# Kernel optimization log

Hardware: AMD Instinct MI355X
Metric: run time of the kernel (lower is better)

Reference implementation:

```python
import jax, jax.numpy as jnp
import numpy as np

HEADS = 16
HEAD_DIM = 64  # embed_size 1024 // 16


def setup_inputs() -> dict:
    key = jax.random.key(0)
    ks = jax.random.split(key, 6)
    N, S, E = 2, 2048, 1024
    return {
        "values": jax.random.normal(ks[0], (N, S, E), dtype=jnp.float32),
        "keys": jax.random.normal(ks[1], (N, S, E), dtype=jnp.float32),
        "queries": jax.random.normal(ks[2], (N, S, E), dtype=jnp.float32),
        "Wv": jax.random.normal(ks[3], (E, E), dtype=jnp.float32) * (E ** -0.5),
        "Wk": jax.random.normal(ks[4], (E, E), dtype=jnp.float32) * (E ** -0.5),
        "Wq": jax.random.normal(ks[5], (E, E), dtype=jnp.float32) * (E ** -0.5),
    }


def reference(values, keys, queries, Wv, Wk, Wq):
    N, Sq, E = queries.shape
    Sk = keys.shape[1]
    H, D = HEADS, HEAD_DIM
    # linear projections (torch Linear: x @ W^T), then split heads
    v = (values @ Wv.T).reshape(N, Sk, H, D)
    k = (keys @ Wk.T).reshape(N, Sk, H, D)
    q = (queries @ Wq.T).reshape(N, Sq, H, D)
    # QK^T -> [N, H, Q, K]
    scores = jnp.einsum("nqhd,nkhd->nhqk", q, k)
    # no mask (original forward takes mask=None path); scale by sqrt(head_dim)
    attn = jax.nn.softmax(scores / jnp.asarray(D, scores.dtype) ** 0.5, axis=-1)
    # AV -> [N, Q, H, D] -> [N, Q, E]; note: fc_out is never applied in the original forward
    out = jnp.einsum("nhql,nlhd->nqhd", attn, v).reshape(N, Sq, H * D)
    return out
```

## Files before the change

### kernel.cpp

```cpp
#include <hip/hip_runtime.h>
#include <math.h>

#define SEQ 2048
#define EMB 1024
#define NH  16
#define HD  64

typedef __attribute__((ext_vector_type(8))) short short8;
typedef __attribute__((ext_vector_type(4))) float f32x4;

static const size_t XE = (size_t)2 * SEQ * EMB;
static const size_t WE = (size_t)EMB * EMB;

static __device__ __forceinline__ short f2bf(float f) {
    unsigned u = __builtin_bit_cast(unsigned, f);
    u = u + 0x7fffu + ((u >> 16) & 1u);
    return (short)(u >> 16);
}

#if __has_builtin(__builtin_amdgcn_cvt_pk_bf16_f32)
typedef __attribute__((ext_vector_type(2))) __bf16 bf16x2;
static __device__ __forceinline__ unsigned pk2(float a, float b) {
    bf16x2 v = __builtin_amdgcn_cvt_pk_bf16_f32(a, b);
    return __builtin_bit_cast(unsigned, v);
}
#else
static __device__ __forceinline__ unsigned pk2(float a, float b) {
    return (unsigned)(unsigned short)f2bf(a) |
           ((unsigned)(unsigned short)f2bf(b) << 16);
}
#endif

static __device__ __forceinline__ short8 cvt8(float4 a, float4 b) {
    union { unsigned u[4]; short8 s; } r;
    r.u[0] = pk2(a.x, a.y); r.u[1] = pk2(a.z, a.w);
    r.u[2] = pk2(b.x, b.y); r.u[3] = pk2(b.z, b.w);
    return r.s;
}

static __device__ __forceinline__ void gload16(const void* g, void* l) {
    __builtin_amdgcn_global_load_lds(
        (const __attribute__((address_space(1))) void*)g,
        (__attribute__((address_space(3))) void*)l, 16, 0, 0);
}

__global__ __launch_bounds__(256)
void cvt_all(const float* __restrict__ xq, const float* __restrict__ xk,
             const float* __restrict__ xv, const float* __restrict__ wq,
             const float* __restrict__ wk, const float* __restrict__ wv,
             short* __restrict__ dxq, short* __restrict__ dxk,
             short* __restrict__ dxv, short* __restrict__ dw) {
    int id = blockIdx.x;
    const float* s; short* d; size_t i;
    if (id < 6144) {
        int seg = id >> 11, o = id & 2047;
        s = (seg == 0) ? xq : (seg == 1) ? xk : xv;
        d = (seg == 0) ? dxq : (seg == 1) ? dxk : dxv;
        i = (size_t)o * 256 + threadIdx.x;
    } else {
        int wid = id - 6144;
        int seg = wid >> 9, o = wid & 511;
        s = (seg == 0) ? wq : (seg == 1) ? wk : wv;
        d = dw + (size_t)seg * WE;
        i = (size_t)o * 256 + threadIdx.x;
    }
    const float4* sp = (const float4*)s;
    float4 a = sp[2 * i], b = sp[2 * i + 1];
    *(short8*)(d + i * 8) = cvt8(a, b);
}

#define ES_STRIDE 136
__global__ __launch_bounds__(256, 4)
void proj(const short* __restrict__ Xq, const short* __restrict__ Xk,
          const short* __restrict__ Xv, const short* __restrict__ Wb,
          short* __restrict__ qb, short* __restrict__ kbuf,
          short* __restrict__ vt) {
    __shared__ __align__(16) char lds_raw[34816];
    short8* Fs = (short8*)lds_raw;
    short8* Hs = (short8*)(lds_raw + 16384);
    short*  Es = (short*)lds_raw;

    const int L = blockIdx.x;
    const int xcd = L & 7, i = L >> 3;
    const int z = i >> 5;
    const int m = i & 31;
    const int ty = xcd * 4 + (m & 3);
    const int tx = m >> 2;

    const short* Fop; const short* Hop; short* C;
    if (z == 0)      { Fop = Xq; Hop = Wb;           C = qb;   }
    else if (z == 1) { Fop = Xk; Hop = Wb + WE;      C = kbuf; }
    else             { Fop = Xv; Hop = Wb + 2 * WE;  C = vt;   }
    const int fr0 = ty * 128;
    const int hr0 = tx * 128;

    const int t = threadIdx.x, w = t >> 6, lane = t & 63;
    const int l15 = lane & 15, quad = lane >> 4;
    const int mh = (w >> 1) * 64, nh2 = (w & 1) * 64;

    auto stageF = [&](int pp, int k0) {
#pragma unroll
        for (int j = 0; j < 2; ++j) {
            int g = j * 256 + t, row = g & 127, c = g >> 7;
            gload16(Fop + (size_t)(fr0 + row) * EMB + k0 + c * 8,
                    &Fs[pp * 512 + j * 256 + w * 64]);
        }
    };
    auto stageH = [&](int pp, int k0) {
#pragma unroll
        for (int j = 0; j < 2; ++j) {
            int g = j * 256 + t, row = g & 127, c = g >> 7;
            gload16(Hop + (size_t)(hr0 + row) * EMB + k0 + c * 8,
                    &Hs[pp * 512 + j * 256 + w * 64]);
        }
    };

    f32x4 acc[4][4];
#pragma unroll
    for (int a = 0; a < 4; ++a)
#pragma unroll
        for (int b = 0; b < 4; ++b) acc[a][b] = 0.f;

    stageF(0, 0);
    stageH(0, 0);

    int p = 0;
    for (int k0 = 0; k0 < EMB; k0 += 32, p ^= 1) {
        __syncthreads();
        if (k0 + 32 < EMB) { stageF(p ^ 1, k0 + 32); stageH(p ^ 1, k0 + 32); }

        short8 af[4], bf[4];
        if (z < 2) {
#pragma unroll
            for (int mi = 0; mi < 4; ++mi)
                af[mi] = Fs[p * 512 + quad * 128 + mh + mi * 16 + l15];
#pragma unroll
            for (int ni = 0; ni < 4; ++ni)
                bf[ni] = Hs[p * 512 + quad * 128 + nh2 + ni * 16 + l15];
        } else {
#pragma unroll
            for (int mi = 0; mi < 4; ++mi)
                af[mi] = Hs[p * 512 + quad * 128 + mh + mi * 16 + l15];
#pragma unroll
            for (int ni = 0; ni < 4; ++ni)
                bf[ni] = Fs[p * 512 + quad * 128 + nh2 + ni * 16 + l15];
        }
#pragma unroll
        for (int mi = 0; mi < 4; ++mi)
#pragma unroll
            for (int ni = 0; ni < 4; ++ni)
                acc[mi][ni] = __builtin_amdgcn_mfma_f32_16x16x32_bf16(
                    af[mi], bf[ni], acc[mi][ni], 0, 0, 0);
    }

    __syncthreads();
#pragma unroll
    for (int mi = 0; mi < 4; ++mi)
#pragma unroll
        for (int ni = 0; ni < 4; ++ni)
#pragma unroll
            for (int r = 0; r < 4; ++r) {
                int lr_ = mh + mi * 16 + quad * 4 + r;
                int lc_ = nh2 + ni * 16 + l15;
                Es[lr_ * ES_STRIDE + lc_] = f2bf(acc[mi][ni][r]);
            }
    __syncthreads();
    {
        int row = t >> 1, half = t & 1;
        const short* src = Es + row * ES_STRIDE + half * 64;
        short* dst;
        if (z < 2) {
            dst = C + (size_t)(fr0 + row) * EMB + hr0 + half * 64;
        } else {
            int bz = fr0 >> 11, s0 = fr0 & 2047;
            dst = C + ((size_t)bz * EMB + hr0 + row) * SEQ + s0 + half * 64;
        }
#pragma unroll
        for (int j = 0; j < 8; ++j)
            *(short8*)(dst + j * 8) = *(const short8*)(src + j * 8);
    }
}

__global__ __launch_bounds__(256, 2)
void attn_mfma(const short* __restrict__ Qg, const short* __restrict__ Kg,
               const short* __restrict__ Vtg, float* __restrict__ OutD) {
    __shared__ short8 QPs[1024];
    __shared__ short8 Ks[2][1024];
    __shared__ short8 Vs[2][1024];

    const int t = threadIdx.x, w = t >> 6, lane = t & 63;
    const int l15 = lane & 15, quad = lane >> 4;
    const int lr3 = lane >> 3, lc7 = lane & 7;
    const int L = blockIdx.x;
    const int xcd = L & 7, i = L >> 3;
    const int bh = xcd * 4 + (i & 3);
    const int q0 = (i >> 2) * 128;
    const int b = bh >> 4, h = bh & 15;
    const short* Qb = Qg + (size_t)b * SEQ * EMB + h * HD;
    const short* Kb = Kg + (size_t)b * SEQ * EMB + h * HD;
    const short* Vb = Vtg + ((size_t)b * EMB + h * HD) * SEQ;

    auto stageKV = [&](int p, int kt) {
#pragma unroll
        for (int j = 0; j < 4; ++j) {
            int rb = w * 32 + j * 8;
            int krow = rb + lr3;
            gload16(Kb + (size_t)(kt + krow) * EMB + ((lc7 ^ (krow & 7)) * 8),
                    &Ks[p][rb * 8]);
            int half = w >> 1, db = (w & 1) * 32 + j * 8;
            int d = db + lr3;
            gload16(Vb + (size_t)d * SEQ + kt + half * 64 + ((lc7 ^ (d & 7)) * 8),
                    &Vs[p][half * 512 + db * 8]);
        }
    };

#pragma unroll
    for (int j = 0; j < 4; ++j) {
        int rb = w * 32 + j * 8;
        int row = rb + lr3;
        gload16(Qb + (size_t)(q0 + row) * EMB + ((lc7 ^ (row & 7)) * 8),
                &QPs[rb * 8]);
    }
    stageKV(0, 0);
    __syncthreads();

    short8 qf[2][2];
#pragma unroll
    for (int qi = 0; qi < 2; ++qi)
#pragma unroll
        for (int kb2 = 0; kb2 < 2; ++kb2) {
            int row = w * 32 + qi * 16 + l15;
            qf[qi][kb2] = QPs[row * 8 + ((kb2 * 4 + quad) ^ (l15 & 7))];
        }

    f32x4 o[2][4];
    float lr[2] = {0.f, 0.f};
#pragma unroll
    for (int qi = 0; qi < 2; ++qi)
#pragma unroll
        for (int ni = 0; ni < 4; ++ni) o[qi][ni] = 0.f;
    const float cl2 = 0.18033688011112042f;
    const float c0  = 11.541560327111707f;

    int p = 0;
    for (int kt = 0; kt < SEQ; kt += 128, p ^= 1) {
        if (kt) __syncthreads();
        if (kt + 128 < SEQ) stageKV(p ^ 1, kt + 128);

#pragma unroll
        for (int half = 0; half < 2; ++half) {
            f32x4 s[4][2];
#pragma unroll
            for (int kblk = 0; kblk < 4; ++kblk)
#pragma unroll
                for (int qi = 0; qi < 2; ++qi) s[kblk][qi] = 0.f;
#pragma unroll
            for (int kb2 = 0; kb2 < 2; ++kb2) {
                short8 ak[4];
#pragma unroll
                for (int kblk = 0; kblk < 4; ++kblk) {
                    int row = half * 64 + kblk * 16 + l15;
                    ak[kblk] = Ks[p][row * 8 + ((kb2 * 4 + quad) ^ (l15 & 7))];
                }
#pragma unroll
                for (int kblk = 0; kblk < 4; ++kblk)
#pragma unroll
                    for (int qi = 0; qi < 2; ++qi)
                        s[kblk][qi] = __builtin_amdgcn_mfma_f32_16x16x32_bf16(
                            ak[kblk], qf[qi][kb2], s[kblk][qi], 0, 0, 0);
            }

#pragma unroll
            for (int qi = 0; qi < 2; ++qi) {
                int row = w * 32 + qi * 16 + l15;
#pragma unroll
                for (int kblk = 0; kblk < 4; ++kblk) {
                    float p0 = __builtin_amdgcn_exp2f(fmaf(s[kblk][qi][0], cl2, -c0));
                    float p1 = __builtin_amdgcn_exp2f(fmaf(s[kblk][qi][1], cl2, -c0));
                    float p2 = __builtin_amdgcn_exp2f(fmaf(s[kblk][qi][2], cl2, -c0));
                    float p3 = __builtin_amdgcn_exp2f(fmaf(s[kblk][qi][3], cl2, -c0));
                    lr[qi] += (p0 + p1) + (p2 + p3);
                    uint2 pv; pv.x = pk2(p0, p1); pv.y = pk2(p2, p3);
                    int kc = kblk * 2 + (quad >> 1);
                    *(uint2*)((char*)QPs +
                        (((row * 8 + (kc ^ (l15 & 7))) << 4) | ((quad & 1) << 3)))
                        = pv;
                }
            }

#pragma unroll
            for (int kb2 = 0; kb2 < 2; ++kb2) {
                short8 ap[2], bv[4];
#pragma unroll
                for (int qi = 0; qi < 2; ++qi) {
                    int row = w * 32 + qi * 16 + l15;
                    ap[qi] = QPs[row * 8 + ((kb2 * 4 + quad) ^ (l15 & 7))];
                }
#pragma unroll
                for (int ni = 0; ni < 4; ++ni) {
                    int dr = ni * 16 + l15;
                    bv[ni] = Vs[p][half * 512 + dr * 8 +
                                   ((kb2 * 4 + quad) ^ (l15 & 7))];
                }
#pragma unroll
                for (int qi = 0; qi < 2; ++qi)
#pragma unroll
                    for (int ni = 0; ni < 4; ++ni)
                        o[qi][ni] = __builtin_amdgcn_mfma_f32_16x16x32_bf16(
                            ap[qi], bv[ni], o[qi][ni], 0, 0, 0);
            }
        }
    }

#pragma unroll
    for (int qi = 0; qi < 2; ++qi) {
        float l = lr[qi];
        l += __shfl_xor(l, 16);
        l += __shfl_xor(l, 32);
        lr[qi] = l;
    }
#pragma unroll
    for (int qi = 0; qi < 2; ++qi)
#pragma unroll
        for (int r = 0; r < 4; ++r) {
            float inv = 1.0f / __shfl(lr[qi], quad * 4 + r);
            int q = q0 + w * 32 + qi * 16 + quad * 4 + r;
            float* op = OutD + ((size_t)b * SEQ + q) * EMB + h * HD;
#pragma unroll
            for (int ni = 0; ni < 4; ++ni)
                op[ni * 16 + l15] = o[qi][ni][r] * inv;
        }
}

extern "C" void kernel_launch(void* const* d_in, const int* in_sizes, int n_in,
                              void* d_out, int out_size, void* d_ws, size_t ws_size,
                              hipStream_t stream) {
    const float* values  = (const float*)d_in[0];
    const float* keys    = (const float*)d_in[1];
    const float* queries = (const float*)d_in[2];
    const float* Wv      = (const float*)d_in[3];
    const float* Wk      = (const float*)d_in[4];
    const float* Wq      = (const float*)d_in[5];
    float* out = (float*)d_out;

    short* qb  = (short*)d_ws;
    short* kb  = qb + XE;
    short* vt  = kb + XE;
    short* wb  = vt + XE;
    short* xqb = wb + 3 * WE;
    short* xkb = xqb + XE;
    short* xvb = xkb + XE;

    cvt_all<<<7680, 256, 0, stream>>>(queries, keys, values, Wq, Wk, Wv,
                                      xqb, xkb, xvb, wb);
    proj<<<768, 256, 0, stream>>>(xqb, xkb, xvb, wb, qb, kb, vt);
    attn_mfma<<<512, 256, 0, stream>>>(qb, kb, vt, out);
}
```

Measured before the change: 214.2 us.

## Use 512-thread projection blocks with K=64 stages and XOR-swizzled LDS

The projection GEMM kernel now runs 512 threads (8 waves) per block, each wave computing a 64x32 sub-tile instead of 64x64. Each stage loads a 64-wide K slice, halving the number of barrier iterations. Shared-memory tiles are stored row-major with an XOR swizzle on the 16-byte chunk index to avoid bank conflicts. In exchange, LDS use roughly doubles to 64KB per block, which may limit resident blocks per CU, and per-wave register tiles shrink, lowering fragment reuse.

```diff
diff --git a/kernel.cpp b/kernel.cpp
--- a/kernel.cpp
+++ b/kernel.cpp
@@ -70,14 +70,14 @@
 }
 
 #define ES_STRIDE 136
-__global__ __launch_bounds__(256, 4)
+__global__ __launch_bounds__(512, 4)
 void proj(const short* __restrict__ Xq, const short* __restrict__ Xk,
           const short* __restrict__ Xv, const short* __restrict__ Wb,
           short* __restrict__ qb, short* __restrict__ kbuf,
           short* __restrict__ vt) {
-    __shared__ __align__(16) char lds_raw[34816];
+    __shared__ __align__(16) char lds_raw[65536];
     short8* Fs = (short8*)lds_raw;
-    short8* Hs = (short8*)(lds_raw + 16384);
+    short8* Hs = (short8*)(lds_raw + 32768);
     short*  Es = (short*)lds_raw;
 
     const int L = blockIdx.x;
@@ -96,87 +96,93 @@
 
     const int t = threadIdx.x, w = t >> 6, lane = t & 63;
     const int l15 = lane & 15, quad = lane >> 4;
-    const int mh = (w >> 1) * 64, nh2 = (w & 1) * 64;
+    const int lr3 = lane >> 3, lc7 = lane & 7;
+    const int mh = (w >> 2) * 64;
+    const int nh = (w & 3) * 32;
 
     auto stageF = [&](int pp, int k0) {
 #pragma unroll
         for (int j = 0; j < 2; ++j) {
-            int g = j * 256 + t, row = g & 127, c = g >> 7;
-            gload16(Fop + (size_t)(fr0 + row) * EMB + k0 + c * 8,
-                    &Fs[pp * 512 + j * 256 + w * 64]);
+            int rb = j * 64 + w * 8;
+            gload16(Fop + (size_t)(fr0 + rb + lr3) * EMB + k0 + ((lc7 ^ lr3) * 8),
+                    &Fs[pp * 1024 + rb * 8]);
         }
     };
     auto stageH = [&](int pp, int k0) {
 #pragma unroll
         for (int j = 0; j < 2; ++j) {
-            int g = j * 256 + t, row = g & 127, c = g >> 7;
-            gload16(Hop + (size_t)(hr0 + row) * EMB + k0 + c * 8,
-                    &Hs[pp * 512 + j * 256 + w * 64]);
+            int rb = j * 64 + w * 8;
+            gload16(Hop + (size_t)(hr0 + rb + lr3) * EMB + k0 + ((lc7 ^ lr3) * 8),
+                    &Hs[pp * 1024 + rb * 8]);
         }
     };
 
-    f32x4 acc[4][4];
+    f32x4 acc[4][2];
 #pragma unroll
     for (int a = 0; a < 4; ++a)
 #pragma unroll
-        for (int b = 0; b < 4; ++b) acc[a][b] = 0.f;
+        for (int b = 0; b < 2; ++b) acc[a][b] = 0.f;
 
     stageF(0, 0);
     stageH(0, 0);
 
     int p = 0;
-    for (int k0 = 0; k0 < EMB; k0 += 32, p ^= 1) {
+    for (int k0 = 0; k0 < EMB; k0 += 64, p ^= 1) {
         __syncthreads();
-        if (k0 + 32 < EMB) { stageF(p ^ 1, k0 + 32); stageH(p ^ 1, k0 + 32); }
-
-        short8 af[4], bf[4];
-        if (z < 2) {
+        if (k0 + 64 < EMB) { stageF(p ^ 1, k0 + 64); stageH(p ^ 1, k0 + 64); }
+
+#pragma unroll
+        for (int kb2 = 0; kb2 < 2; ++kb2) {
+            short8 af[4], bf[2];
+            int cx = (kb2 * 4 + quad) ^ (l15 & 7);
+            if (z < 2) {
+#pragma unroll
+                for (int mi = 0; mi < 4; ++mi)
+                    af[mi] = Fs[p * 1024 + (mh + mi * 16 + l15) * 8 + cx];
+#pragma unroll
+                for (int ni = 0; ni < 2; ++ni)
+                    bf[ni] = Hs[p * 1024 + (nh + ni * 16 + l15) * 8 + cx];
+            } else {
+#pragma unroll
+                for (int mi = 0; mi < 4; ++mi)
+                    af[mi] = Hs[p * 1024 + (mh + mi * 16 + l15) * 8 + cx];
+#pragma unroll
+                for (int ni = 0; ni < 2; ++ni)
+                    bf[ni] = Fs[p * 1024 + (nh + ni * 16 + l15) * 8 + cx];
+            }
 #pragma unroll
             for (int mi = 0; mi < 4; ++mi)
-                af[mi] = Fs[p * 512 + quad * 128 + mh + mi * 16 + l15];
-#pragma unroll
-            for (int ni = 0; ni < 4; ++ni)
-                bf[ni] = Hs[p * 512 + quad * 128 + nh2 + ni * 16 + l15];
-        } else {
-#pragma unroll
-            for (int mi = 0; mi < 4; ++mi)
-                af[mi] = Hs[p * 512 + quad * 128 + mh + mi * 16 + l15];
-#pragma unroll
-            for (int ni = 0; ni < 4; ++ni)
-                bf[ni] = Fs[p * 512 + quad * 128 + nh2 + ni * 16 + l15];
-        }
-#pragma unroll
-        for (int mi = 0; mi < 4; ++mi)
-#pragma unroll
-            for (int ni = 0; ni < 4; ++ni)
-                acc[mi][ni] = __builtin_amdgcn_mfma_f32_16x16x32_bf16(
-                    af[mi], bf[ni], acc[mi][ni], 0, 0, 0);
+#pragma unroll
+                for (int ni = 0; ni < 2; ++ni)
+                    acc[mi][ni] = __builtin_amdgcn_mfma_f32_16x16x32_bf16(
+                        af[mi], bf[ni], acc[mi][ni], 0, 0, 0);
+        }
     }
 
     __syncthreads();
 #pragma unroll
     for (int mi = 0; mi < 4; ++mi)
 #pragma unroll
-        for (int ni = 0; ni < 4; ++ni)
+        for (int ni = 0; ni < 2; ++ni)
 #pragma unroll
             for (int r = 0; r < 4; ++r) {
                 int lr_ = mh + mi * 16 + quad * 4 + r;
-                int lc_ = nh2 + ni * 16 + l15;
+                int lc_ = nh + ni * 16 + l15;
                 Es[lr_ * ES_STRIDE + lc_] = f2bf(acc[mi][ni][r]);
             }
     __syncthreads();
     {
-        int row = t >> 1, half = t & 1;
-        const short* src = Es + row * ES_STRIDE + half * 64;
+        int row = t >> 2, q4 = t & 3;
+        const short* src = Es + row * ES_STRIDE + q4 * 32;
         short* dst;
         if (z < 2) {
-            dst = C + (size_t)(fr0 + row) * EMB + hr0 + half * 64;
+            dst = C + (size_t)(fr0 + row) * EMB + hr0 + q4 * 32;
         } else {
             int bz = fr0 >> 11, s0 = fr0 & 2047;
-            dst = C + ((size_t)bz * EMB + hr0 + row) * SEQ + s0 + half * 64;
-        }
-#pragma unroll
-        for (int j = 0; j < 8; ++j)
+            dst = C + ((size_t)bz * EMB + hr0 + row) * SEQ + s0 + q4 * 32;
+        }
+#pragma unroll
+        for (int j = 0; j < 4; ++j)
             *(short8*)(dst + j * 8) = *(const short8*)(src + j * 8);
     }
 }
@@ -353,6 +359,6 @@
 
     cvt_all<<<7680, 256, 0, stream>>>(queries, keys, values, Wq, Wk, Wv,
                                       xqb, xkb, xvb, wb);
-    proj<<<768, 256, 0, stream>>>(xqb, xkb, xvb, wb, qb, kb, vt);
+    proj<<<768, 512, 0, stream>>>(xqb, xkb, xvb, wb, qb, kb, vt);
     attn_mfma<<<512, 256, 0, stream>>>(qb, kb, vt, out);
 }
```

Result: faster. 188.9 us (-11.8%).
